# Optimization experiments

Measured on AMD Instinct MI355X. Metric: run time of the kernel, lower is better.

The kernel has to match this reference:

```python
import jax, jax.numpy as jnp
import numpy as np

B, T, OBS, ACT, H, OUT, NLAYERS = 4096, 50, 64, 16, 256, 64, 5


def setup_inputs() -> dict:
    key = jax.random.key(0)
    ks = jax.random.split(key, 8)
    w = 0.05
    return {
        "trajectory": jax.random.normal(ks[0], (B, T, OBS), dtype=jnp.float32),
        "actions": jax.random.normal(ks[1], (B, T, ACT), dtype=jnp.float32),
        "Wi": jax.random.normal(ks[2], (OBS + ACT, 4 * H), dtype=jnp.float32) * w,
        "Wh": jax.random.normal(ks[3], (H, 4 * H), dtype=jnp.float32) * w,
        "bh": jnp.zeros((4 * H,), dtype=jnp.float32),
        "mlp_W": jax.random.normal(ks[4], (NLAYERS, H, H), dtype=jnp.float32) * w,
        "mlp_b": jnp.zeros((NLAYERS, H), dtype=jnp.float32),
        "Wout": jax.random.normal(ks[5], (H, OUT), dtype=jnp.float32) * w,
        "bout": jnp.zeros((OUT,), dtype=jnp.float32),
    }


def reference(trajectory, actions, Wi, Wh, bh, mlp_W, mlp_b, Wout, bout):
    # Features extractor = flatten (identity for 1D sensor obs); preprocess is identity for Box.
    x = jnp.concatenate([trajectory, actions], axis=-1)  # [B, T, OBS+ACT]
    xs = jnp.swapaxes(x, 0, 1)  # [T, B, D] for scan over time

    hdim = Wh.shape[0]
    c0 = jnp.zeros((x.shape[0], hdim), dtype=x.dtype)
    h0 = jnp.zeros((x.shape[0], hdim), dtype=x.dtype)

    def step(carry, xt):
        c, h = carry
        z = xt @ Wi + h @ Wh + bh  # [B, 4H]
        zi, zf, zg, zo = jnp.split(z, 4, axis=-1)
        i = jax.nn.sigmoid(zi)
        f = jax.nn.sigmoid(zf)
        g = jax.nn.silu(zg)  # activation_fn=nn.silu
        o = jax.nn.sigmoid(zo)
        c_new = f * c + i * g
        h_new = o * jax.nn.silu(c_new)
        return (c_new, h_new), None

    (c, h), _ = jax.lax.scan(step, (c0, h0), xs)

    out = h
    for k in range(mlp_W.shape[0]):
        out = jax.nn.silu(out @ mlp_W[k] + mlp_b[k])
    pred = out @ Wout + bout
    return pred
```

## Files before the change

kernel.cpp:

```cpp
#include <hip/hip_runtime.h>
#include <hip/hip_fp16.h>


typedef _Float16 h8 __attribute__((ext_vector_type(8)));
typedef _Float16 hv4 __attribute__((ext_vector_type(4)));
typedef float f4 __attribute__((ext_vector_type(4)));

#define NB    4096
#define TSEQ  50
#define DOBS  64
#define DACT  16
#define HD    256
#define DOUT  64
#define NL    5

#define NKT   11
#define AROW  360
#define MTILE 16
#define NWG   (NB / MTILE)
#define NTHR  512

#define WS_MLP   (704 * 512)
#define WS_WOUT  (WS_MLP + 640 * 512)

#define LDS_AS     (MTILE * AROW)
#define LDS_WCOFF  (2 * LDS_AS)
#define WCB        16
#define LDS_HALVES (LDS_WCOFF + 8 * WCB * 512)
#define LDS_BYTES  (LDS_HALVES * 2)
static_assert(LDS_BYTES <= 160 * 1024, "LDS overflow");

#define SB_P     12
#define NSTREAM  44

__device__ __forceinline__ float sigf(float x) {
  const float e = __builtin_amdgcn_exp2f(x * -1.44269504088896f);
  return __builtin_amdgcn_rcpf(1.f + e);
}

__device__ constexpr int soff(int c) {
  const int g = c & 3, kt = c >> 2;
  return (((g * 16 + 1) * NKT) + kt) * 512;
}

__global__ void __launch_bounds__(256) repack_kernel(
    const float* __restrict__ Wi, const float* __restrict__ Wh,
    const float* __restrict__ mlpW, const float* __restrict__ Wout,
    _Float16* __restrict__ wsW)
{
  const int gt  = blockIdx.x * 256 + threadIdx.x;
  const int gb  = gt >> 6;
  const int l   = gt & 63;
  const int l15 = l & 15;
  const int kb  = (l >> 4) * 8;
  h8 v;
  if (gb < 704) {
    const int nt = gb / NKT, kt = gb - nt * NKT;
    const int n  = nt * 16 + l15;
#pragma unroll
    for (int j = 0; j < 8; ++j) {
      const int k = kt * 32 + kb + j;
      float s = 0.f;
      if (k < 80)       s = Wi[k * 1024 + n];
      else if (k < 336) s = Wh[(k - 80) * 1024 + n];
      v[j] = (_Float16)s;
    }
  } else if (gb < 1344) {
    const int b2 = gb - 704;
    const int L  = b2 >> 7, rr = b2 & 127;
    const int nt = rr >> 3, kt = rr & 7;
    const int n  = nt * 16 + l15;
#pragma unroll
    for (int j = 0; j < 8; ++j) {
      const int k = kt * 32 + kb + j;
      v[j] = (_Float16)mlpW[(size_t)L * 65536 + k * 256 + n];
    }
  } else {
    const int b3 = gb - 1344;
    const int nt = b3 >> 3, kt = b3 & 7;
    const int n  = nt * 16 + l15;
#pragma unroll
    for (int j = 0; j < 8; ++j) {
      const int k = kt * 32 + kb + j;
      v[j] = (_Float16)Wout[k * 64 + n];
    }
  }
  *(h8*)&wsW[(size_t)gb * 512 + l * 8] = v;
}

__global__ void __launch_bounds__(NTHR, 2) lstm_kernel(
    const float* __restrict__ traj, const float* __restrict__ acts,
    const float* __restrict__ bh,   const float* __restrict__ mlpb,
    const float* __restrict__ bout, const _Float16* __restrict__ wsW,
    float* __restrict__ out)
{
  extern __shared__ __align__(16) _Float16 lds[];
  _Float16* As0 = lds;
  _Float16* As1 = lds + LDS_AS;
  _Float16* Wc  = lds + LDS_WCOFF;

  const int tid = threadIdx.x;
  const int w   = tid >> 6;
  const int l   = tid & 63;
  const int l15 = l & 15;
  const int lq  = l >> 4;
  const int rbase = blockIdx.x * MTILE;

  for (int i = tid; i < 2 * LDS_AS; i += NTHR) lds[i] = (_Float16)0.f;

#pragma unroll
  for (int j = 0; j < WCB; ++j) {
    const int g = j & 3, kt = 7 + (j >> 2);
    const h8 v = *(const h8*)&wsW[(size_t)((g * 16 + w * 2) * NKT + kt) * 512 + l * 8];
    *(h8*)&Wc[(w * WCB + j) * 512 + l * 8] = v;
  }

  h8 rw[28];
#pragma unroll
  for (int kt = 0; kt < 7; ++kt)
#pragma unroll
    for (int g = 0; g < 4; ++g)
      rw[kt * 4 + g] = *(const h8*)&wsW[(size_t)((g * 16 + w * 2) * NKT + kt) * 512 + l * 8];

  float c[2][4];
#pragma unroll
  for (int cb = 0; cb < 2; ++cb)
#pragma unroll
    for (int r = 0; r < 4; ++r) c[cb][r] = 0.f;

  float bias[4][2];
#pragma unroll
  for (int g = 0; g < 4; ++g) {
    bias[g][0] = bh[g * 256 + w * 32 + l15];
    bias[g][1] = bh[g * 256 + w * 32 + 16 + l15];
  }

  __syncthreads();

  if (tid < 256) {
    const int r = tid >> 4, q = tid & 15;
    const float4 v = *(const float4*)&traj[(size_t)(rbase + r) * (TSEQ * DOBS) + q * 4];
    hv4 hx = { (_Float16)v.x, (_Float16)v.y, (_Float16)v.z, (_Float16)v.w };
    *(hv4*)&As0[r * AROW + q * 4] = hx;
  } else {
    const int r = (tid - 256) >> 4, q = (tid - 256) & 15;
    As0[r * AROW + 64 + q] = (_Float16)acts[(size_t)(rbase + r) * (TSEQ * DACT) + q];
  }
  __syncthreads();

  unsigned long long wbits = (unsigned long long)(const void*)wsW;

  auto step = [&](int t, const _Float16* buf, _Float16* nbuf) {
    asm volatile("" : "+s"(wbits) : : "memory");
    const _Float16* wst = (const _Float16*)wbits;
    const _Float16* wlb = wst + (size_t)(w * 2 * NKT) * 512 + l * 8;

    float4 xv; float xa;
    const bool havex = (t + 1 < TSEQ);
    if (havex) {
      if (tid < 256) {
        const int r = tid >> 4, q = tid & 15;
        xv = *(const float4*)&traj[(size_t)(rbase + r) * (TSEQ * DOBS) + (t + 1) * DOBS + q * 4];
      } else {
        const int r = (tid - 256) >> 4, q = (tid - 256) & 15;
        xa = acts[(size_t)(rbase + r) * (TSEQ * DACT) + (t + 1) * DACT + q];
      }
    }

    h8 sb[SB_P];
#pragma unroll
    for (int cc = 0; cc < SB_P; ++cc) sb[cc] = *(const h8*)&wlb[soff(cc)];

    {
      f4 acc[4];
#pragma unroll
      for (int g = 0; g < 4; ++g) acc[g] = f4{0.f, 0.f, 0.f, 0.f};
#pragma unroll
      for (int kt = 0; kt < NKT; ++kt) {
        const h8 a0 = *(const h8*)&buf[l15 * AROW + kt * 32 + lq * 8];
#pragma unroll
        for (int g = 0; g < 4; ++g) {
          h8 bf;
          if (kt < 7) bf = rw[kt * 4 + g];
          else        bf = *(const h8*)&Wc[(w * WCB + (kt - 7) * 4 + g) * 512 + l * 8];
          acc[g] = __builtin_amdgcn_mfma_f32_16x16x32_f16(a0, bf, acc[g], 0, 0, 0);
        }
      }
      const int colh = 80 + w * 32 + l15;
#pragma unroll
      for (int r = 0; r < 4; ++r) {
        const float zi = acc[0][r] + bias[0][0];
        const float zf = acc[1][r] + bias[1][0];
        const float zg = acc[2][r] + bias[2][0];
        const float zo = acc[3][r] + bias[3][0];
        const float ig = sigf(zi), fg = sigf(zf), og = sigf(zo);
        const float gg = zg * sigf(zg);
        const float cn = fg * c[0][r] + ig * gg;
        c[0][r] = cn;
        nbuf[(lq * 4 + r) * AROW + colh] = (_Float16)(og * cn * sigf(cn));
      }
    }

    {
      f4 acc[4];
#pragma unroll
      for (int g = 0; g < 4; ++g) acc[g] = f4{0.f, 0.f, 0.f, 0.f};
#pragma unroll
      for (int kt = 0; kt < NKT; ++kt) {
        const h8 a0 = *(const h8*)&buf[l15 * AROW + kt * 32 + lq * 8];
#pragma unroll
        for (int g = 0; g < 4; ++g) {
          const int cc = kt * 4 + g;
          const int s  = cc % SB_P;
          const h8 bf = sb[s];
          acc[g] = __builtin_amdgcn_mfma_f32_16x16x32_f16(a0, bf, acc[g], 0, 0, 0);
          if (cc + SB_P < NSTREAM) sb[s] = *(const h8*)&wlb[soff(cc + SB_P)];
        }
      }
      const int colh = 80 + w * 32 + 16 + l15;
#pragma unroll
      for (int r = 0; r < 4; ++r) {
        const float zi = acc[0][r] + bias[0][1];
        const float zf = acc[1][r] + bias[1][1];
        const float zg = acc[2][r] + bias[2][1];
        const float zo = acc[3][r] + bias[3][1];
        const float ig = sigf(zi), fg = sigf(zf), og = sigf(zo);
        const float gg = zg * sigf(zg);
        const float cn = fg * c[1][r] + ig * gg;
        c[1][r] = cn;
        nbuf[(lq * 4 + r) * AROW + colh] = (_Float16)(og * cn * sigf(cn));
      }
    }

    if (havex) {
      if (tid < 256) {
        const int r = tid >> 4, q = tid & 15;
        hv4 hx = { (_Float16)xv.x, (_Float16)xv.y, (_Float16)xv.z, (_Float16)xv.w };
        *(hv4*)&nbuf[r * AROW + q * 4] = hx;
      } else {
        const int r = (tid - 256) >> 4, q = (tid - 256) & 15;
        nbuf[r * AROW + 64 + q] = (_Float16)xa;
      }
    }
  };

#pragma unroll 1
  for (int t = 0; t < TSEQ; t += 2) {
    step(t, As0, As1);
    __syncthreads();
    step(t + 1, As1, As0);
    __syncthreads();
  }

  for (int i = tid; i < MTILE * HD; i += NTHR) {
    const int r = i >> 8, cc = i & 255;
    As1[r * AROW + cc] = As0[r * AROW + 80 + cc];
  }
  __syncthreads();

#pragma unroll 1
  for (int L = 0; L < NL; ++L) {
    const _Float16* in = (L & 1) ? As0 : As1;
    _Float16*       ob = (L & 1) ? As1 : As0;
    const _Float16* wl = wsW + WS_MLP + (size_t)L * (128 * 512);
    float bcol[2];
    bcol[0] = mlpb[L * HD + w * 32 + l15];
    bcol[1] = mlpb[L * HD + w * 32 + 16 + l15];

    f4 acc[2];
    acc[0] = f4{0.f, 0.f, 0.f, 0.f};
    acc[1] = f4{0.f, 0.f, 0.f, 0.f};
#pragma unroll
    for (int kt = 0; kt < 8; ++kt) {
      const h8 a0 = *(const h8*)&in[l15 * AROW + kt * 32 + lq * 8];
#pragma unroll
      for (int cb = 0; cb < 2; ++cb) {
        const h8 bf = *(const h8*)&wl[(size_t)((w * 2 + cb) * 8 + kt) * 512 + l * 8];
        acc[cb] = __builtin_amdgcn_mfma_f32_16x16x32_f16(a0, bf, acc[cb], 0, 0, 0);
      }
    }
#pragma unroll
    for (int cb = 0; cb < 2; ++cb)
#pragma unroll
      for (int r = 0; r < 4; ++r) {
        const float z = acc[cb][r] + bcol[cb];
        ob[(lq * 4 + r) * AROW + w * 32 + cb * 16 + l15] = (_Float16)(z * sigf(z));
      }
    __syncthreads();
  }

  if (w < 4) {
    const _Float16* wo = wsW + WS_WOUT;
    const float bo = bout[w * 16 + l15];
    f4 acc0 = f4{0.f, 0.f, 0.f, 0.f};
#pragma unroll
    for (int kt = 0; kt < 8; ++kt) {
      const h8 a0 = *(const h8*)&As0[l15 * AROW + kt * 32 + lq * 8];
      const h8 bf = *(const h8*)&wo[(size_t)(w * 8 + kt) * 512 + l * 8];
      acc0 = __builtin_amdgcn_mfma_f32_16x16x32_f16(a0, bf, acc0, 0, 0, 0);
    }
#pragma unroll
    for (int r = 0; r < 4; ++r)
      out[(size_t)(rbase + lq * 4 + r) * DOUT + w * 16 + l15] = acc0[r] + bo;
  }
}

extern "C" void kernel_launch(void* const* d_in, const int* in_sizes, int n_in,
                              void* d_out, int out_size, void* d_ws, size_t ws_size,
                              hipStream_t stream)
{
  const float* traj = (const float*)d_in[0];
  const float* acts = (const float*)d_in[1];
  const float* Wi   = (const float*)d_in[2];
  const float* Wh   = (const float*)d_in[3];
  const float* bh   = (const float*)d_in[4];
  const float* mlpW = (const float*)d_in[5];
  const float* mlpb = (const float*)d_in[6];
  const float* Wout = (const float*)d_in[7];
  const float* bout = (const float*)d_in[8];
  _Float16* wsW = (_Float16*)d_ws;

  (void)hipFuncSetAttribute((const void*)lstm_kernel,
                            hipFuncAttributeMaxDynamicSharedMemorySize, LDS_BYTES);

  repack_kernel<<<344, 256, 0, stream>>>(Wi, Wh, mlpW, Wout, wsW);
  lstm_kernel<<<NWG, NTHR, LDS_BYTES, stream>>>(traj, acts, bh, mlpb, bout, wsW, (float*)d_out);
}
```

Baseline: 337.0 us.

## Interleave both hidden-half gate GEMMs in one k-loop, rebalancing weight residency

The two back-to-back MFMA loops per timestep, one for each 16-column half of the hidden state, are merged into a single k-loop. Each A-fragment load now feeds two independent accumulator chains, which exposes more MFMA-level parallelism and removes one pass of LDS A reads. To free registers for the second accumulator set, the first half keeps one fewer k-tile of weights in registers. One more tile moves into LDS, and the last k-tile of the first half is streamed from global through the existing rotating prefetch buffer (NSTREAM 44→48). The trade-off is extra global weight traffic per step and higher register pressure that could cause spills.

```diff
diff --git a/kernel.cpp b/kernel.cpp
--- a/kernel.cpp
+++ b/kernel.cpp
@@ -31,7 +31,7 @@
 static_assert(LDS_BYTES <= 160 * 1024, "LDS overflow");
 
 #define SB_P     12
-#define NSTREAM  44
+#define NSTREAM  48
 
 __device__ __forceinline__ float sigf(float x) {
   const float e = __builtin_amdgcn_exp2f(x * -1.44269504088896f);
@@ -39,8 +39,8 @@
 }
 
 __device__ constexpr int soff(int c) {
-  const int g = c & 3, kt = c >> 2;
-  return (((g * 16 + 1) * NKT) + kt) * 512;
+  if (c < 44) { const int g = c & 3, kt = c >> 2; return ((g * 16 + 1) * NKT + kt) * 512; }
+  const int g = c - 44; return ((g * 16) * NKT + 10) * 512;
 }
 
 __global__ void __launch_bounds__(256) repack_kernel(
@@ -110,14 +110,14 @@
 
 #pragma unroll
   for (int j = 0; j < WCB; ++j) {
-    const int g = j & 3, kt = 7 + (j >> 2);
+    const int g = j & 3, kt = 6 + (j >> 2);
     const h8 v = *(const h8*)&wsW[(size_t)((g * 16 + w * 2) * NKT + kt) * 512 + l * 8];
     *(h8*)&Wc[(w * WCB + j) * 512 + l * 8] = v;
   }
 
-  h8 rw[28];
-#pragma unroll
-  for (int kt = 0; kt < 7; ++kt)
+  h8 rw[24];
+#pragma unroll
+  for (int kt = 0; kt < 6; ++kt)
 #pragma unroll
     for (int g = 0; g < 4; ++g)
       rw[kt * 4 + g] = *(const h8*)&wsW[(size_t)((g * 16 + w * 2) * NKT + kt) * 512 + l * 8];
@@ -171,28 +171,38 @@
 #pragma unroll
     for (int cc = 0; cc < SB_P; ++cc) sb[cc] = *(const h8*)&wlb[soff(cc)];
 
+    f4 acc0[4], acc1[4];
+#pragma unroll
+    for (int g = 0; g < 4; ++g) {
+      acc0[g] = f4{0.f, 0.f, 0.f, 0.f};
+      acc1[g] = f4{0.f, 0.f, 0.f, 0.f};
+    }
+
+#pragma unroll
+    for (int kt = 0; kt < NKT; ++kt) {
+      const h8 a0 = *(const h8*)&buf[l15 * AROW + kt * 32 + lq * 8];
+#pragma unroll
+      for (int g = 0; g < 4; ++g) {
+        h8 bf0;
+        if (kt < 6)       bf0 = rw[kt * 4 + g];
+        else if (kt < 10) bf0 = *(const h8*)&Wc[(w * WCB + (kt - 6) * 4 + g) * 512 + l * 8];
+        else              bf0 = sb[(44 + g) % SB_P];
+        acc0[g] = __builtin_amdgcn_mfma_f32_16x16x32_f16(a0, bf0, acc0[g], 0, 0, 0);
+
+        const int cc = kt * 4 + g;
+        acc1[g] = __builtin_amdgcn_mfma_f32_16x16x32_f16(a0, sb[cc % SB_P], acc1[g], 0, 0, 0);
+        if (cc + SB_P < NSTREAM) sb[cc % SB_P] = *(const h8*)&wlb[soff(cc + SB_P)];
+      }
+    }
+
     {
-      f4 acc[4];
-#pragma unroll
-      for (int g = 0; g < 4; ++g) acc[g] = f4{0.f, 0.f, 0.f, 0.f};
-#pragma unroll
-      for (int kt = 0; kt < NKT; ++kt) {
-        const h8 a0 = *(const h8*)&buf[l15 * AROW + kt * 32 + lq * 8];
-#pragma unroll
-        for (int g = 0; g < 4; ++g) {
-          h8 bf;
-          if (kt < 7) bf = rw[kt * 4 + g];
-          else        bf = *(const h8*)&Wc[(w * WCB + (kt - 7) * 4 + g) * 512 + l * 8];
-          acc[g] = __builtin_amdgcn_mfma_f32_16x16x32_f16(a0, bf, acc[g], 0, 0, 0);
-        }
-      }
       const int colh = 80 + w * 32 + l15;
 #pragma unroll
       for (int r = 0; r < 4; ++r) {
-        const float zi = acc[0][r] + bias[0][0];
-        const float zf = acc[1][r] + bias[1][0];
-        const float zg = acc[2][r] + bias[2][0];
-        const float zo = acc[3][r] + bias[3][0];
+        const float zi = acc0[0][r] + bias[0][0];
+        const float zf = acc0[1][r] + bias[1][0];
+        const float zg = acc0[2][r] + bias[2][0];
+        const float zo = acc0[3][r] + bias[3][0];
         const float ig = sigf(zi), fg = sigf(zf), og = sigf(zo);
         const float gg = zg * sigf(zg);
         const float cn = fg * c[0][r] + ig * gg;
@@ -200,30 +210,14 @@
         nbuf[(lq * 4 + r) * AROW + colh] = (_Float16)(og * cn * sigf(cn));
       }
     }
-
     {
-      f4 acc[4];
-#pragma unroll
-      for (int g = 0; g < 4; ++g) acc[g] = f4{0.f, 0.f, 0.f, 0.f};
-#pragma unroll
-      for (int kt = 0; kt < NKT; ++kt) {
-        const h8 a0 = *(const h8*)&buf[l15 * AROW + kt * 32 + lq * 8];
-#pragma unroll
-        for (int g = 0; g < 4; ++g) {
-          const int cc = kt * 4 + g;
-          const int s  = cc % SB_P;
-          const h8 bf = sb[s];
-          acc[g] = __builtin_amdgcn_mfma_f32_16x16x32_f16(a0, bf, acc[g], 0, 0, 0);
-          if (cc + SB_P < NSTREAM) sb[s] = *(const h8*)&wlb[soff(cc + SB_P)];
-        }
-      }
       const int colh = 80 + w * 32 + 16 + l15;
 #pragma unroll
       for (int r = 0; r < 4; ++r) {
-        const float zi = acc[0][r] + bias[0][1];
-        const float zf = acc[1][r] + bias[1][1];
-        const float zg = acc[2][r] + bias[2][1];
-        const float zo = acc[3][r] + bias[3][1];
+        const float zi = acc1[0][r] + bias[0][1];
+        const float zf = acc1[1][r] + bias[1][1];
+        const float zg = acc1[2][r] + bias[2][1];
+        const float zo = acc1[3][r] + bias[3][1];
         const float ig = sigf(zi), fg = sigf(zf), og = sigf(zo);
         const float gg = zg * sigf(zg);
         const float cn = fg * c[1][r] + ig * gg;
```

Result: slower. 385.5 us (+14.4%).
